# Kernel optimization log

Measured on AMD Instinct MI355X. Metric: run time of the kernel, lower is better.

The kernel has to match this reference:

```python
import jax, jax.numpy as jnp
import numpy as np

B, DIM, HW = 16, 256, 64      # input feature map
G, DH = 8, 64                 # offset_groups = heads = 8, dim_head = 64
DPG = DIM // G                # 32 channels per group
TP = 8                        # tile size: 8x8 grid of 8x8 tiles
DS = 4                        # downsample factor -> 2x2 offset grid per tile
CPB_DIM = DIM // 4            # 64, CPB mlp width
SCALE = DH ** -0.5


def _grid_sample(img, grid):
    # F.grid_sample, bilinear, zero padding, align_corners=False
    # img (N,C,H,W), grid (N,Ho,Wo,2) with last dim (x,y) in [-1,1]
    N, C, H, W = img.shape
    Ho, Wo = grid.shape[1:3]
    x = ((grid[..., 0] + 1.0) * W - 1.0) / 2.0
    y = ((grid[..., 1] + 1.0) * H - 1.0) / 2.0
    x0 = jnp.floor(x)
    y0 = jnp.floor(y)
    imgf = img.reshape(N, C, H * W)
    out = jnp.zeros((N, C, Ho * Wo), img.dtype)
    for dx, wx in ((0.0, x0 + 1.0 - x), (1.0, x - x0)):
        for dy, wy in ((0.0, y0 + 1.0 - y), (1.0, y - y0)):
            ix = x0 + dx
            iy = y0 + dy
            valid = (ix >= 0) & (ix < W) & (iy >= 0) & (iy < H)
            idx = (jnp.clip(iy, 0, H - 1) * W + jnp.clip(ix, 0, W - 1)).astype(jnp.int32)
            idxf = idx.reshape(N, Ho * Wo)
            g = jax.vmap(lambda im, ii: im[:, ii])(imgf, idxf)  # (N,C,HoWo)
            w = (wx * wy * valid).reshape(N, 1, Ho * Wo)
            out = out + g * w
    return out.reshape(N, C, Ho, Wo)


def _forward(x, ln_g, ln_b, wq, wk, wv, off_w1, off_b1, off_w2,
             cpb_w1, cpb_b1, cpb_w2, cpb_b2, cpb_w3, cpb_b3, wo, bo):
    Bb, C, H, W = x.shape
    # LayerNorm over channel dim (eps=1e-6)
    xt = jnp.moveaxis(x, 1, -1)
    mu = xt.mean(-1, keepdims=True)
    var = ((xt - mu) ** 2).mean(-1, keepdims=True)
    xt = (xt - mu) * jax.lax.rsqrt(var + 1e-6) * ln_g + ln_b
    x = jnp.moveaxis(xt, -1, 1)
    # patchify: (b c (i p) (j q)) -> ((i j b) c p q)  [vectorizes the 64-iter python loop]
    xp = x.reshape(Bb, C, 8, TP, 8, TP).transpose(2, 4, 0, 1, 3, 5).reshape(64 * Bb, C, TP, TP)
    N = 64 * Bb
    # grouped 1x1 to_q (groups = offset_groups)
    xg = xp.reshape(N, G, DPG, TP, TP)
    q = jnp.einsum('ngchw,goc->ngohw', xg, wq)          # (N,8,64,8,8)
    gq = q.reshape(N * G, DH, TP, TP)
    # offset net: depthwise conv k=6 s=4 p=1 -> GELU -> 1x1 -> tanh -> *offset_scale
    off = jax.lax.conv_general_dilated(gq, off_w1, (DS, DS), ((1, 1), (1, 1)),
                                       feature_group_count=DH)
    off = jax.nn.gelu(off + off_b1[None, :, None, None], approximate=False)
    off = jnp.tanh(jnp.einsum('nchw,oc->nohw', off, off_w2)) * float(DS)  # (N*G,2,2,2)
    # virtual sampling grid on the 2x2 offset grid, normalized by (size-1)
    r = jnp.arange(2, dtype=x.dtype)
    gx, gy = jnp.meshgrid(r, r, indexing='xy')
    vgrid = jnp.stack([gx, gy])[None] + off              # (N*G,2,2,2) ch=(x,y)
    vnorm = 2.0 * vgrid - 1.0                            # max(2-1,1)=1
    vgrid_s = jnp.moveaxis(vnorm, 1, -1)                 # (N*G,2,2,2) last=(x,y)
    kv = _grid_sample(xp.reshape(N * G, DPG, TP, TP), vgrid_s)   # (N*G,32,2,2)
    kvf = kv.reshape(N, G, DPG, 2, 2)
    k = jnp.einsum('ngchw,goc->ngohw', kvf, wk)          # (N,8,64,2,2)
    v = jnp.einsum('ngchw,goc->ngohw', kvf, wv)
    qh = q.transpose(0, 1, 3, 4, 2).reshape(N, G, TP * TP, DH) * SCALE
    kh = k.transpose(0, 1, 3, 4, 2).reshape(N, G, 4, DH)
    vh = v.transpose(0, 1, 3, 4, 2).reshape(N, G, 4, DH)
    sim = jnp.einsum('bhid,bhjd->bhij', qh, kh)          # (N,8,64,4)
    # continuous position bias (CPB)
    rq = jnp.arange(TP, dtype=x.dtype)
    qx, qy = jnp.meshgrid(rq, rq, indexing='xy')
    gridq = jnp.stack([qx, qy], -1).reshape(TP * TP, 2) * (2.0 / (TP - 1)) - 1.0
    pos = gridq[None, :, None, :] - vgrid_s.reshape(N * G, 1, 4, 2)  # (N*G,64,4,2)
    bz = jnp.sign(pos) * jnp.log1p(jnp.abs(pos))
    bz = jax.nn.relu(bz @ cpb_w1 + cpb_b1)
    bz = jax.nn.relu(bz @ cpb_w2 + cpb_b2)
    bz = (bz @ cpb_w3 + cpb_b3).reshape(N, G, TP * TP, 4)
    attn = jax.nn.softmax(sim + bz, axis=-1)
    out = jnp.einsum('bhij,bhjd->bhid', attn, vh)        # (N,8,64,64)
    out = out.transpose(0, 1, 3, 2).reshape(N, G * DH, TP, TP)
    out = jnp.einsum('nchw,oc->nohw', out, wo) + bo[None, :, None, None]
    # reassemble: ((i j b) c p q) -> (b c (i p) (j q))
    y = out.reshape(8, 8, Bb, C, TP, TP).transpose(2, 3, 0, 4, 1, 5).reshape(Bb, C, H, W)
    return y


def setup_inputs() -> dict:
    key = jax.random.key(0)
    ks = jax.random.split(key, 12)
    s = 0.05
    return {
        'x': jax.random.normal(ks[0], (B, DIM, HW, HW), jnp.float32),
        'ln_g': jnp.ones((DIM,), jnp.float32),
        'ln_b': jnp.zeros((DIM,), jnp.float32),
        'wq': jax.random.normal(ks[1], (G, DH, DPG), jnp.float32) * s,
        'wk': jax.random.normal(ks[2], (G, DH, DPG), jnp.float32) * s,
        'wv': jax.random.normal(ks[3], (G, DH, DPG), jnp.float32) * s,
        'off_w1': jax.random.normal(ks[4], (DH, 1, 6, 6), jnp.float32) * s,
        'off_b1': jnp.zeros((DH,), jnp.float32),
        'off_w2': jax.random.normal(ks[5], (2, DH), jnp.float32) * s,
        'cpb_w1': jax.random.normal(ks[6], (2, CPB_DIM), jnp.float32) * s,
        'cpb_b1': jnp.zeros((CPB_DIM,), jnp.float32),
        'cpb_w2': jax.random.normal(ks[7], (CPB_DIM, CPB_DIM), jnp.float32) * s,
        'cpb_b2': jnp.zeros((CPB_DIM,), jnp.float32),
        'cpb_w3': jax.random.normal(ks[8], (CPB_DIM, 1), jnp.float32) * s,
        'cpb_b3': jnp.zeros((1,), jnp.float32),
        'wo': jax.random.normal(ks[9], (DIM, G * DH), jnp.float32) * s,
        'bo': jnp.zeros((DIM,), jnp.float32),
    }


def reference(x, ln_g, ln_b, wq, wk, wv, off_w1, off_b1, off_w2,
              cpb_w1, cpb_b1, cpb_w2, cpb_b2, cpb_w3, cpb_b3, wo, bo):
    return _forward(x, ln_g, ln_b, wq, wk, wv, off_w1, off_b1, off_w2,
                    cpb_w1, cpb_b1, cpb_w2, cpb_b2, cpb_w3, cpb_b3, wo, bo)
```

## Files before the change

### kernel.cpp

```cpp
#include <hip/hip_runtime.h>
#include <math.h>


#define WS_VN  16777216
#define WS_WOT 16842752

typedef __attribute__((ext_vector_type(8))) short short8;
typedef __attribute__((ext_vector_type(4))) short short4b;
typedef __attribute__((ext_vector_type(4))) float f32x4;

__device__ __forceinline__ short f2bf(float f) {
  unsigned u = __builtin_bit_cast(unsigned, f);
  u += 0x7fff + ((u >> 16) & 1);
  return (short)(u >> 16);
}
__device__ __forceinline__ float bf2f(short h) {
  return __builtin_bit_cast(float, ((unsigned)(unsigned short)h) << 16);
}

__global__ __launch_bounds__(256) void k1_ln(const float* __restrict__ x,
    const float* __restrict__ ln_g, const float* __restrict__ ln_b,
    float* __restrict__ xn) {
  int blk = blockIdx.x;
  int b = blk >> 6, h = blk & 63;
  int t = threadIdx.x;
  int quarter = t >> 6, wcol = t & 63;
  const float* xrow = x + (size_t)b * (256 * 4096) + h * 64 + wcol;
  float vv[64];
  float s = 0.f, ss = 0.f;
#pragma unroll
  for (int i = 0; i < 64; ++i) {
    float v = xrow[(size_t)(quarter * 64 + i) * 4096];
    vv[i] = v; s += v; ss += v * v;
  }
  __shared__ float sm[4][64], sq[4][64], mu_s[64], rs_s[64];
  sm[quarter][wcol] = s; sq[quarter][wcol] = ss;
  __syncthreads();
  if (t < 64) {
    float S  = sm[0][t] + sm[1][t] + sm[2][t] + sm[3][t];
    float SS = sq[0][t] + sq[1][t] + sq[2][t] + sq[3][t];
    float mu = S * (1.f / 256.f);
    float var = SS * (1.f / 256.f) - mu * mu;
    mu_s[t] = mu;
    rs_s[t] = 1.f / sqrtf(var + 1e-6f);
  }
  __syncthreads();
  float mu = mu_s[wcol], rs = rs_s[wcol];
  int it = h >> 3, p = h & 7, jt = wcol >> 3, qq = wcol & 7;
  int n = (it * 8 + jt) * 16 + b;
  int pos = p * 8 + qq;
  float* xo = xn + (size_t)n * 16384 + pos * 256 + quarter * 64;
#pragma unroll
  for (int i = 0; i < 64; i += 4) {
    float4 o4;
    o4.x = (vv[i + 0] - mu) * rs * ln_g[quarter * 64 + i + 0] + ln_b[quarter * 64 + i + 0];
    o4.y = (vv[i + 1] - mu) * rs * ln_g[quarter * 64 + i + 1] + ln_b[quarter * 64 + i + 1];
    o4.z = (vv[i + 2] - mu) * rs * ln_g[quarter * 64 + i + 2] + ln_b[quarter * 64 + i + 2];
    o4.w = (vv[i + 3] - mu) * rs * ln_g[quarter * 64 + i + 3] + ln_b[quarter * 64 + i + 3];
    *(float4*)&xo[i] = o4;
  }
}

__global__ __launch_bounds__(256) void k0_cvt(const float* __restrict__ wo,
    short* __restrict__ woH, short* __restrict__ woL,
    const float* __restrict__ wq,
    short* __restrict__ wqH, short* __restrict__ wqL,
    const float* __restrict__ cw2, short* __restrict__ bfragG) {
  int blk = blockIdx.x;
  if (blk < 512) {
    int idx = blk * 256 + threadIdx.x;
    float v = wo[idx];
    short hi = f2bf(v);
    woH[idx] = hi;
    woL[idx] = f2bf(v - bf2f(hi));
  } else if (blk < 576) {
    int idx = (blk - 512) * 256 + threadIdx.x;
    float v = wq[idx];
    short hi = f2bf(v);
    wqH[idx] = hi;
    wqL[idx] = f2bf(v - bf2f(hi));
  } else {
    int t = threadIdx.x;
#pragma unroll
    for (int rep = 0; rep < 2; ++rep) {
      int slot = t + rep * 256;
      int combo = slot >> 6, ln = slot & 63;
      int kstep = combo >> 2, nt = combo & 3;
      int kbase = kstep * 32 + (ln >> 4) * 8;
      int ncol = nt * 16 + (ln & 15);
      short8 v;
#pragma unroll
      for (int jj = 0; jj < 8; ++jj) v[jj] = f2bf(cw2[(kbase + jj) * 64 + ncol]);
      *(short8*)&bfragG[slot * 8] = v;
    }
  }
}

__global__ __launch_bounds__(256, 4) void k2_qoff(const float* __restrict__ xn,
    const short* __restrict__ wqH, const short* __restrict__ wqL,
    const float* __restrict__ w1, const float* __restrict__ b1,
    const float* __restrict__ w2, short* __restrict__ qb,
    float* __restrict__ vn) {
  int blk = blockIdx.x;
  int n = blk >> 1, gh = blk & 1;
  int w = threadIdx.x >> 6;
  int lane = threadIdx.x & 63;
  int l15 = lane & 15, q4 = lane >> 4;
  __shared__ float qs[64][65];

  const float* w1c = w1 + lane * 36;
  float b1v = b1[lane];
  float w2a = w2[lane];
  float w2b = w2[64 + lane];
  int oy = w >> 1, ox = w & 1;
  int posc = w * 16 + l15;

  for (int gi = 0; gi < 4; ++gi) {
    int g = gh * 4 + gi;
    int ng = n * 8 + g;
    const float* xb = xn + (size_t)n * 16384 + posc * 256 + g * 32 + q4 * 8;
    float4 v0 = *(const float4*)xb;
    float4 v1 = *(const float4*)(xb + 4);
    float vj[8] = {v0.x, v0.y, v0.z, v0.w, v1.x, v1.y, v1.z, v1.w};
    short8 BH, BL;
#pragma unroll
    for (int j = 0; j < 8; ++j) {
      float v = vj[j];
      short hi = f2bf(v);
      BH[j] = hi;
      BL[j] = f2bf(v - bf2f(hi));
    }
    const short* wqHg = wqH + g * 2048;
    const short* wqLg = wqL + g * 2048;
    short* qrow = qb + ((size_t)(n * 64 + posc) * 512 + g * 64);
#pragma unroll
    for (int mt = 0; mt < 4; ++mt) {
      short8 AH = *(const short8*)&wqHg[(mt * 16 + l15) * 32 + q4 * 8];
      short8 AL = *(const short8*)&wqLg[(mt * 16 + l15) * 32 + q4 * 8];
      f32x4 acc = {0.f, 0.f, 0.f, 0.f};
      acc = __builtin_amdgcn_mfma_f32_16x16x32_bf16(AH, BH, acc, 0, 0, 0);
      acc = __builtin_amdgcn_mfma_f32_16x16x32_bf16(AL, BH, acc, 0, 0, 0);
      acc = __builtin_amdgcn_mfma_f32_16x16x32_bf16(AH, BL, acc, 0, 0, 0);
      int obase = mt * 16 + q4 * 4;
#pragma unroll
      for (int reg = 0; reg < 4; ++reg) qs[obase + reg][posc] = acc[reg];
      short4b qv;
#pragma unroll
      for (int reg = 0; reg < 4; ++reg) qv[reg] = f2bf(acc[reg]);
      *(short4b*)&qrow[obase] = qv;
    }
    __syncthreads();
    float a = 0.f;
#pragma unroll
    for (int ky = 0; ky < 6; ++ky) {
      int iy = oy * 4 - 1 + ky;
      if (iy < 0 || iy > 7) continue;
#pragma unroll
      for (int kx = 0; kx < 6; ++kx) {
        int ix = ox * 4 - 1 + kx;
        if (ix < 0 || ix > 7) continue;
        a += w1c[ky * 6 + kx] * qs[lane][iy * 8 + ix];
      }
    }
    a += b1v;
    a = 0.5f * a * (1.f + erff(a * 0.70710678118654752f));
    float p0 = w2a * a, p1 = w2b * a;
#pragma unroll
    for (int st = 1; st < 64; st <<= 1) {
      p0 += __shfl_xor(p0, st, 64);
      p1 += __shfl_xor(p1, st, 64);
    }
    if (lane == 0) {
      float offx = tanhf(p0) * 4.f;
      float offy = tanhf(p1) * 4.f;
      float2 o2;
      o2.x = 2.f * ((float)ox + offx) - 1.f;
      o2.y = 2.f * ((float)oy + offy) - 1.f;
      *(float2*)&vn[(size_t)ng * 8 + w * 2] = o2;
    }
    __syncthreads();
  }
}

__global__ __launch_bounds__(256, 3) void k3_attn(const float* __restrict__ xn,
    const float* __restrict__ wk, const float* __restrict__ wv,
    const float* __restrict__ vn, const short* __restrict__ bfragG,
    const float* __restrict__ cw1, const float* __restrict__ cb1,
    const float* __restrict__ cb2,
    const float* __restrict__ cw3, const float* __restrict__ cb3,
    short* __restrict__ qattB) {
  int w = threadIdx.x >> 6;
  int lane = threadIdx.x & 63;
  int ng = blockIdx.x * 4 + w;
  int n = ng >> 3, g = ng & 7;
  __shared__ alignas(16) float kvs[4][32][4];
  __shared__ alignas(16) float ks[4][64][4];
  __shared__ alignas(16) float vs[4][64][4];
  __shared__ alignas(16) short bfragLDS[512 * 8];
  __shared__ float biasS[4][4][64];

  {
    int t = threadIdx.x;
    *(short8*)&bfragLDS[t * 8]         = *(const short8*)&bfragG[t * 8];
    *(short8*)&bfragLDS[(t + 256) * 8] = *(const short8*)&bfragG[(t + 256) * 8];
  }

  const float* vp = vn + (size_t)ng * 8;
  float4 vp0 = *(const float4*)vp;
  float4 vp1 = *(const float4*)(vp + 4);
  float vx0 = vp0.x, vy0 = vp0.y, vx1 = vp0.z, vy1 = vp0.w;
  float vx2 = vp1.x, vy2 = vp1.y, vx3 = vp1.z, vy3 = vp1.w;
  {
    int c = lane & 31, s2 = lane >> 5;
    const float* tile = xn + (size_t)n * 16384 + g * 32 + c;
#pragma unroll
    for (int rep = 0; rep < 2; ++rep) {
      int s = s2 + 2 * rep;
      float vxs = (rep == 0) ? (s2 ? vx1 : vx0) : (s2 ? vx3 : vx2);
      float vys = (rep == 0) ? (s2 ? vy1 : vy0) : (s2 ? vy3 : vy2);
      float X = 4.f * vxs + 3.5f, Y = 4.f * vys + 3.5f;
      float x0f = floorf(X), y0f = floorf(Y);
      int x0 = (int)x0f, y0 = (int)y0f;
      float wx1 = X - x0f, wy1 = Y - y0f;
      float acc = 0.f;
      for (int dy = 0; dy < 2; ++dy) {
        int iy = y0 + dy;
        if (iy < 0 || iy > 7) continue;
        float wyv = dy ? wy1 : 1.f - wy1;
        for (int dx = 0; dx < 2; ++dx) {
          int ix = x0 + dx;
          if (ix < 0 || ix > 7) continue;
          float wxv = dx ? wx1 : 1.f - wx1;
          acc += tile[(iy * 8 + ix) * 256] * wxv * wyv;
        }
      }
      kvs[w][c][s] = acc;
    }
  }
  __syncthreads();
  {
    int d = lane;
    float ka0 = 0, ka1 = 0, ka2 = 0, ka3 = 0, va0 = 0, va1 = 0, va2 = 0, va3 = 0;
    const float4* wk4 = (const float4*)(wk + g * 2048 + d * 32);
    const float4* wv4 = (const float4*)(wv + g * 2048 + d * 32);
#pragma unroll
    for (int c4 = 0; c4 < 8; ++c4) {
      float4 a4 = wk4[c4], b4 = wv4[c4];
      float aw[4] = {a4.x, a4.y, a4.z, a4.w};
      float bw[4] = {b4.x, b4.y, b4.z, b4.w};
#pragma unroll
      for (int u = 0; u < 4; ++u) {
        float4 kv4 = *(const float4*)kvs[w][c4 * 4 + u];
        ka0 += aw[u] * kv4.x; ka1 += aw[u] * kv4.y;
        ka2 += aw[u] * kv4.z; ka3 += aw[u] * kv4.w;
        va0 += bw[u] * kv4.x; va1 += bw[u] * kv4.y;
        va2 += bw[u] * kv4.z; va3 += bw[u] * kv4.w;
      }
    }
    ks[w][d][0] = ka0; ks[w][d][1] = ka1; ks[w][d][2] = ka2; ks[w][d][3] = ka3;
    vs[w][d][0] = va0; vs[w][d][1] = va1; vs[w][d][2] = va2; vs[w][d][3] = va3;
  }
  __syncthreads();
  float sim0 = 0, sim1 = 0, sim2 = 0, sim3 = 0;
  short* qrow = qattB + ((size_t)(n * 64 + lane) * 512 + g * 64);
#pragma unroll 2
  for (int d8 = 0; d8 < 8; ++d8) {
    short8 q8 = *(const short8*)&qrow[d8 * 8];
#pragma unroll
    for (int j = 0; j < 8; ++j) {
      float qv = bf2f(q8[j]);
      float4 k4 = *(const float4*)ks[w][d8 * 8 + j];
      sim0 += qv * k4.x; sim1 += qv * k4.y; sim2 += qv * k4.z; sim3 += qv * k4.w;
    }
  }
  float logit0 = sim0 * 0.125f, logit1 = sim1 * 0.125f;
  float logit2 = sim2 * 0.125f, logit3 = sim3 * 0.125f;

  short8 bf[2][4];
#pragma unroll
  for (int kstep = 0; kstep < 2; ++kstep)
#pragma unroll
    for (int nt = 0; nt < 4; ++nt)
      bf[kstep][nt] = *(const short8*)&bfragLDS[((kstep * 4 + nt) * 64 + lane) * 8];
  int kcol = (lane >> 4) * 8;
  float c1x[16], c1y[16], c1b[16];
#pragma unroll
  for (int ks2 = 0; ks2 < 2; ++ks2)
#pragma unroll
    for (int jj = 0; jj < 8; ++jj) {
      int i = ks2 * 32 + kcol + jj;
      c1x[ks2 * 8 + jj] = cw1[i];
      c1y[ks2 * 8 + jj] = cw1[64 + i];
      c1b[ks2 * 8 + jj] = cb1[i];
    }
  int jme = lane & 15;
  float w3v[4], b2v[4];
#pragma unroll
  for (int nt = 0; nt < 4; ++nt) {
    w3v[nt] = cw3[nt * 16 + jme];
    b2v[nt] = cb2[nt * 16 + jme];
  }
  float gqx = (float)(jme & 7) * (2.f / 7.f) - 1.f;
  float yrow = (float)(jme >> 3);
#pragma unroll 1
  for (int s = 0; s < 4; ++s) {
    float vxs = (s == 0) ? vx0 : (s == 1) ? vx1 : (s == 2) ? vx2 : vx3;
    float vys = (s == 0) ? vy0 : (s == 1) ? vy1 : (s == 2) ? vy2 : vy3;
    float px = gqx - vxs;
    float tx = copysignf(log1pf(fabsf(px)), px);
    float pre[16];
#pragma unroll
    for (int t2 = 0; t2 < 16; ++t2) pre[t2] = fmaf(tx, c1x[t2], c1b[t2]);
#pragma unroll 1
    for (int mt4 = 0; mt4 < 4; ++mt4) {
      float gqy = (float)(mt4 * 2) * (2.f / 7.f) + yrow * (2.f / 7.f) - 1.f;
      float py = gqy - vys;
      float ty = copysignf(log1pf(fabsf(py)), py);
      short8 af[2];
#pragma unroll
      for (int ks2 = 0; ks2 < 2; ++ks2)
#pragma unroll
        for (int jj = 0; jj < 8; ++jj) {
          float h = fmaxf(fmaf(ty, c1y[ks2 * 8 + jj], pre[ks2 * 8 + jj]), 0.f);
          af[ks2][jj] = f2bf(h);
        }
      f32x4 a0 = {0,0,0,0}, a1 = {0,0,0,0}, a2 = {0,0,0,0}, a3 = {0,0,0,0};
      a0 = __builtin_amdgcn_mfma_f32_16x16x32_bf16(af[0], bf[0][0], a0, 0, 0, 0);
      a0 = __builtin_amdgcn_mfma_f32_16x16x32_bf16(af[1], bf[1][0], a0, 0, 0, 0);
      a1 = __builtin_amdgcn_mfma_f32_16x16x32_bf16(af[0], bf[0][1], a1, 0, 0, 0);
      a1 = __builtin_amdgcn_mfma_f32_16x16x32_bf16(af[1], bf[1][1], a1, 0, 0, 0);
      a2 = __builtin_amdgcn_mfma_f32_16x16x32_bf16(af[0], bf[0][2], a2, 0, 0, 0);
      a2 = __builtin_amdgcn_mfma_f32_16x16x32_bf16(af[1], bf[1][2], a2, 0, 0, 0);
      a3 = __builtin_amdgcn_mfma_f32_16x16x32_bf16(af[0], bf[0][3], a3, 0, 0, 0);
      a3 = __builtin_amdgcn_mfma_f32_16x16x32_bf16(af[1], bf[1][3], a3, 0, 0, 0);
      float part[4];
#pragma unroll
      for (int reg = 0; reg < 4; ++reg) {
        part[reg] = w3v[0] * fmaxf(a0[reg] + b2v[0], 0.f)
                  + w3v[1] * fmaxf(a1[reg] + b2v[1], 0.f)
                  + w3v[2] * fmaxf(a2[reg] + b2v[2], 0.f)
                  + w3v[3] * fmaxf(a3[reg] + b2v[3], 0.f);
      }
#pragma unroll
      for (int st = 1; st < 16; st <<= 1)
#pragma unroll
        for (int reg = 0; reg < 4; ++reg)
          part[reg] += __shfl_xor(part[reg], st, 64);
      if (jme == 0) {
        int posO = mt4 * 16 + (lane >> 4) * 4;
#pragma unroll
        for (int reg = 0; reg < 4; ++reg) biasS[w][s][posO + reg] = part[reg];
      }
    }
  }
  __syncthreads();
  float c3 = cb3[0];
  logit0 += biasS[w][0][lane] + c3;
  logit1 += biasS[w][1][lane] + c3;
  logit2 += biasS[w][2][lane] + c3;
  logit3 += biasS[w][3][lane] + c3;
  float m = fmaxf(fmaxf(logit0, logit1), fmaxf(logit2, logit3));
  float e0 = expf(logit0 - m), e1 = expf(logit1 - m);
  float e2 = expf(logit2 - m), e3 = expf(logit3 - m);
  float inv = 1.f / (e0 + e1 + e2 + e3);
  e0 *= inv; e1 *= inv; e2 *= inv; e3 *= inv;
#pragma unroll 2
  for (int d8 = 0; d8 < 8; ++d8) {
    short8 o8;
#pragma unroll
    for (int j = 0; j < 8; ++j) {
      float4 v4 = *(const float4*)vs[w][d8 * 8 + j];
      o8[j] = f2bf(e0 * v4.x + e1 * v4.y + e2 * v4.z + e3 * v4.w);
    }
    *(short8*)&qrow[d8 * 8] = o8;
  }
}

__global__ __launch_bounds__(256) void k4_mfma(const short* __restrict__ attB,
    const short* __restrict__ woH, const short* __restrict__ woL,
    const float* __restrict__ bo, float* __restrict__ y) {
  int blk = blockIdx.x;
  int b = blk & 15, it = (blk >> 4) & 7, p = blk >> 7;
  int wv = threadIdx.x >> 6;
  int lane = threadIdx.x & 63;
  int mr = lane & 15, kq = (lane >> 4) * 8;
  f32x4 acc[4][4];
#pragma unroll
  for (int mt = 0; mt < 4; ++mt)
#pragma unroll
    for (int nt = 0; nt < 4; ++nt) acc[mt][nt] = (f32x4){0.f, 0.f, 0.f, 0.f};
  int ncol0 = wv * 64 + mr;
  size_t arow[4];
#pragma unroll
  for (int mt = 0; mt < 4; ++mt) {
    int w0 = mt * 16 + mr;
    int jt = w0 >> 3, q = w0 & 7;
    arow[mt] = ((size_t)((it * 8 + jt) * 16 + b) * 64 + p * 8 + q) * 512;
  }
#pragma unroll 2
  for (int kst = 0; kst < 16; ++kst) {
    int k0 = kst * 32 + kq;
    short8 a[4];
#pragma unroll
    for (int mt = 0; mt < 4; ++mt)
      a[mt] = *(const short8*)&attB[arow[mt] + k0];
#pragma unroll
    for (int nt = 0; nt < 4; ++nt) {
      size_t off = (size_t)(ncol0 + nt * 16) * 512 + k0;
      short8 bhi = *(const short8*)&woH[off];
      short8 blo = *(const short8*)&woL[off];
#pragma unroll
      for (int mt = 0; mt < 4; ++mt) {
        acc[mt][nt] = __builtin_amdgcn_mfma_f32_16x16x32_bf16(a[mt], bhi, acc[mt][nt], 0, 0, 0);
        acc[mt][nt] = __builtin_amdgcn_mfma_f32_16x16x32_bf16(a[mt], blo, acc[mt][nt], 0, 0, 0);
      }
    }
  }
#pragma unroll
  for (int nt = 0; nt < 4; ++nt) {
    int o = wv * 64 + nt * 16 + mr;
    float bov = bo[o];
    size_t ybase = ((size_t)b * 256 + o) * 4096 + (it * 8 + p) * 64;
#pragma unroll
    for (int mt = 0; mt < 4; ++mt) {
      int w0 = mt * 16 + (lane >> 4) * 4;
      float4 o4;
      o4.x = acc[mt][nt][0] + bov;
      o4.y = acc[mt][nt][1] + bov;
      o4.z = acc[mt][nt][2] + bov;
      o4.w = acc[mt][nt][3] + bov;
      *(float4*)&y[ybase + w0] = o4;
    }
  }
}

extern "C" void kernel_launch(void* const* d_in, const int* in_sizes, int n_in,
                              void* d_out, int out_size, void* d_ws, size_t ws_size,
                              hipStream_t stream) {
  (void)in_sizes; (void)n_in; (void)out_size; (void)ws_size;
  const float* x    = (const float*)d_in[0];
  const float* ln_g = (const float*)d_in[1];
  const float* ln_b = (const float*)d_in[2];
  const float* wq   = (const float*)d_in[3];
  const float* wk   = (const float*)d_in[4];
  const float* wv   = (const float*)d_in[5];
  const float* ow1  = (const float*)d_in[6];
  const float* ob1  = (const float*)d_in[7];
  const float* ow2  = (const float*)d_in[8];
  const float* cw1  = (const float*)d_in[9];
  const float* cb1  = (const float*)d_in[10];
  const float* cw2  = (const float*)d_in[11];
  const float* cb2  = (const float*)d_in[12];
  const float* cw3  = (const float*)d_in[13];
  const float* cb3  = (const float*)d_in[14];
  const float* wo   = (const float*)d_in[15];
  const float* bo   = (const float*)d_in[16];
  float* y  = (float*)d_out;
  float* ws = (float*)d_ws;
  short* qattB = (short*)ws;
  float* vnb   = ws + WS_VN;
  short* woH   = (short*)(ws + WS_WOT);
  short* woL   = woH + 131072;
  short* wqH   = woL + 131072;
  short* wqL   = wqH + 16384;
  short* bfragG = wqL + 16384;
  float* xn = y;

  k0_cvt<<<577, 256, 0, stream>>>(wo, woH, woL, wq, wqH, wqL, cw2, bfragG);
  k1_ln<<<1024, 256, 0, stream>>>(x, ln_g, ln_b, xn);
  k2_qoff<<<2048, 256, 0, stream>>>(xn, wqH, wqL, ow1, ob1, ow2, qattB, vnb);
  k3_attn<<<2048, 256, 0, stream>>>(xn, wk, wv, vnb, bfragG, cw1, cb1, cb2,
                                    cw3, cb3, qattB);
  k4_mfma<<<1024, 256, 0, stream>>>(qattB, woH, woL, bo, y);
}
```

Measured before the change: 400.9 us.

## Split attention kernel into separate CPB bias kernel and attention kernel

Moves the continuous position bias MLP (MFMA-based) into its own kernel that writes per-head bias to workspace, and reduces the attention kernel to sampling, k/v projection, softmax and output. The split lowers LDS and register pressure in each kernel, so occupancy can rise (launch bounds 4 for attention). It costs an extra launch and a round trip of the bias buffer through global memory. The old fused kernel is kept as a fallback when the workspace is too small.

```diff
diff --git a/kernel.cpp b/kernel.cpp
--- a/kernel.cpp
+++ b/kernel.cpp
@@ -182,13 +182,103 @@
   }
 }
 
-__global__ __launch_bounds__(256, 3) void k3_attn(const float* __restrict__ xn,
-    const float* __restrict__ wk, const float* __restrict__ wv,
-    const float* __restrict__ vn, const short* __restrict__ bfragG,
+__global__ __launch_bounds__(256, 3) void k3a_cpb(const float* __restrict__ vn,
+    const short* __restrict__ bfragG,
     const float* __restrict__ cw1, const float* __restrict__ cb1,
     const float* __restrict__ cb2,
-    const float* __restrict__ cw3, const float* __restrict__ cb3,
-    short* __restrict__ qattB) {
+    const float* __restrict__ cw3, float* __restrict__ biasG) {
+  int w = threadIdx.x >> 6;
+  int lane = threadIdx.x & 63;
+  int ng = blockIdx.x * 4 + w;
+  const float* vp = vn + (size_t)ng * 8;
+  float4 vp0 = *(const float4*)vp;
+  float4 vp1 = *(const float4*)(vp + 4);
+  float vx0 = vp0.x, vy0 = vp0.y, vx1 = vp0.z, vy1 = vp0.w;
+  float vx2 = vp1.x, vy2 = vp1.y, vx3 = vp1.z, vy3 = vp1.w;
+
+  short8 bf[2][4];
+#pragma unroll
+  for (int kstep = 0; kstep < 2; ++kstep)
+#pragma unroll
+    for (int nt = 0; nt < 4; ++nt)
+      bf[kstep][nt] = *(const short8*)&bfragG[((kstep * 4 + nt) * 64 + lane) * 8];
+  int kcol = (lane >> 4) * 8;
+  float c1x[16], c1y[16], c1b[16];
+#pragma unroll
+  for (int ks2 = 0; ks2 < 2; ++ks2)
+#pragma unroll
+    for (int jj = 0; jj < 8; ++jj) {
+      int i = ks2 * 32 + kcol + jj;
+      c1x[ks2 * 8 + jj] = cw1[i];
+      c1y[ks2 * 8 + jj] = cw1[64 + i];
+      c1b[ks2 * 8 + jj] = cb1[i];
+    }
+  int jme = lane & 15;
+  float w3v[4], b2v[4];
+#pragma unroll
+  for (int nt = 0; nt < 4; ++nt) {
+    w3v[nt] = cw3[nt * 16 + jme];
+    b2v[nt] = cb2[nt * 16 + jme];
+  }
+  float gqx = (float)(jme & 7) * (2.f / 7.f) - 1.f;
+  float yrow = (float)(jme >> 3);
+#pragma unroll 1
+  for (int s = 0; s < 4; ++s) {
+    float vxs = (s == 0) ? vx0 : (s == 1) ? vx1 : (s == 2) ? vx2 : vx3;
+    float vys = (s == 0) ? vy0 : (s == 1) ? vy1 : (s == 2) ? vy2 : vy3;
+    float px = gqx - vxs;
+    float tx = copysignf(log1pf(fabsf(px)), px);
+    float pre[16];
+#pragma unroll
+    for (int t2 = 0; t2 < 16; ++t2) pre[t2] = fmaf(tx, c1x[t2], c1b[t2]);
+#pragma unroll 1
+    for (int mt4 = 0; mt4 < 4; ++mt4) {
+      float gqy = (float)(mt4 * 2) * (2.f / 7.f) + yrow * (2.f / 7.f) - 1.f;
+      float py = gqy - vys;
+      float ty = copysignf(log1pf(fabsf(py)), py);
+      short8 af[2];
+#pragma unroll
+      for (int ks2 = 0; ks2 < 2; ++ks2)
+#pragma unroll
+        for (int jj = 0; jj < 8; ++jj) {
+          float h = fmaxf(fmaf(ty, c1y[ks2 * 8 + jj], pre[ks2 * 8 + jj]), 0.f);
+          af[ks2][jj] = f2bf(h);
+        }
+      f32x4 a0 = {0,0,0,0}, a1 = {0,0,0,0}, a2 = {0,0,0,0}, a3 = {0,0,0,0};
+      a0 = __builtin_amdgcn_mfma_f32_16x16x32_bf16(af[0], bf[0][0], a0, 0, 0, 0);
+      a0 = __builtin_amdgcn_mfma_f32_16x16x32_bf16(af[1], bf[1][0], a0, 0, 0, 0);
+      a1 = __builtin_amdgcn_mfma_f32_16x16x32_bf16(af[0], bf[0][1], a1, 0, 0, 0);
+      a1 = __builtin_amdgcn_mfma_f32_16x16x32_bf16(af[1], bf[1][1], a1, 0, 0, 0);
+      a2 = __builtin_amdgcn_mfma_f32_16x16x32_bf16(af[0], bf[0][2], a2, 0, 0, 0);
+      a2 = __builtin_amdgcn_mfma_f32_16x16x32_bf16(af[1], bf[1][2], a2, 0, 0, 0);
+      a3 = __builtin_amdgcn_mfma_f32_16x16x32_bf16(af[0], bf[0][3], a3, 0, 0, 0);
+      a3 = __builtin_amdgcn_mfma_f32_16x16x32_bf16(af[1], bf[1][3], a3, 0, 0, 0);
+      float part[4];
+#pragma unroll
+      for (int reg = 0; reg < 4; ++reg) {
+        part[reg] = w3v[0] * fmaxf(a0[reg] + b2v[0], 0.f)
+                  + w3v[1] * fmaxf(a1[reg] + b2v[1], 0.f)
+                  + w3v[2] * fmaxf(a2[reg] + b2v[2], 0.f)
+                  + w3v[3] * fmaxf(a3[reg] + b2v[3], 0.f);
+      }
+#pragma unroll
+      for (int st = 1; st < 16; st <<= 1)
+#pragma unroll
+        for (int reg = 0; reg < 4; ++reg)
+          part[reg] += __shfl_xor(part[reg], st, 64);
+      if (jme == 0) {
+        int posO = mt4 * 16 + (lane >> 4) * 4;
+        float4 o4 = {part[0], part[1], part[2], part[3]};
+        *(float4*)&biasG[(size_t)ng * 256 + s * 64 + posO] = o4;
+      }
+    }
+  }
+}
+
+__global__ __launch_bounds__(256, 4) void k3b_attn(const float* __restrict__ xn,
+    const float* __restrict__ wk, const float* __restrict__ wv,
+    const float* __restrict__ vn, const float* __restrict__ biasG,
+    const float* __restrict__ cb3, short* __restrict__ qattB) {
   int w = threadIdx.x >> 6;
   int lane = threadIdx.x & 63;
   int ng = blockIdx.x * 4 + w;
@@ -196,14 +286,6 @@
   __shared__ alignas(16) float kvs[4][32][4];
   __shared__ alignas(16) float ks[4][64][4];
   __shared__ alignas(16) float vs[4][64][4];
-  __shared__ alignas(16) short bfragLDS[512 * 8];
-  __shared__ float biasS[4][4][64];
-
-  {
-    int t = threadIdx.x;
-    *(short8*)&bfragLDS[t * 8]         = *(const short8*)&bfragG[t * 8];
-    *(short8*)&bfragLDS[(t + 256) * 8] = *(const short8*)&bfragG[(t + 256) * 8];
-  }
 
   const float* vp = vn + (size_t)ng * 8;
   float4 vp0 = *(const float4*)vp;
@@ -275,6 +357,122 @@
   }
   float logit0 = sim0 * 0.125f, logit1 = sim1 * 0.125f;
   float logit2 = sim2 * 0.125f, logit3 = sim3 * 0.125f;
+  float c3 = cb3[0];
+  const float* bg = biasG + (size_t)ng * 256;
+  logit0 += bg[0 * 64 + lane] + c3;
+  logit1 += bg[1 * 64 + lane] + c3;
+  logit2 += bg[2 * 64 + lane] + c3;
+  logit3 += bg[3 * 64 + lane] + c3;
+  float m = fmaxf(fmaxf(logit0, logit1), fmaxf(logit2, logit3));
+  float e0 = expf(logit0 - m), e1 = expf(logit1 - m);
+  float e2 = expf(logit2 - m), e3 = expf(logit3 - m);
+  float inv = 1.f / (e0 + e1 + e2 + e3);
+  e0 *= inv; e1 *= inv; e2 *= inv; e3 *= inv;
+#pragma unroll 2
+  for (int d8 = 0; d8 < 8; ++d8) {
+    short8 o8;
+#pragma unroll
+    for (int j = 0; j < 8; ++j) {
+      float4 v4 = *(const float4*)vs[w][d8 * 8 + j];
+      o8[j] = f2bf(e0 * v4.x + e1 * v4.y + e2 * v4.z + e3 * v4.w);
+    }
+    *(short8*)&qrow[d8 * 8] = o8;
+  }
+}
+
+__global__ __launch_bounds__(256, 3) void k3_attn(const float* __restrict__ xn,
+    const float* __restrict__ wk, const float* __restrict__ wv,
+    const float* __restrict__ vn, const short* __restrict__ bfragG,
+    const float* __restrict__ cw1, const float* __restrict__ cb1,
+    const float* __restrict__ cb2,
+    const float* __restrict__ cw3, const float* __restrict__ cb3,
+    short* __restrict__ qattB) {
+  int w = threadIdx.x >> 6;
+  int lane = threadIdx.x & 63;
+  int ng = blockIdx.x * 4 + w;
+  int n = ng >> 3, g = ng & 7;
+  __shared__ alignas(16) float kvs[4][32][4];
+  __shared__ alignas(16) float ks[4][64][4];
+  __shared__ alignas(16) float vs[4][64][4];
+  __shared__ alignas(16) short bfragLDS[512 * 8];
+  __shared__ float biasS[4][4][64];
+
+  {
+    int t = threadIdx.x;
+    *(short8*)&bfragLDS[t * 8]         = *(const short8*)&bfragG[t * 8];
+    *(short8*)&bfragLDS[(t + 256) * 8] = *(const short8*)&bfragG[(t + 256) * 8];
+  }
+
+  const float* vp = vn + (size_t)ng * 8;
+  float4 vp0 = *(const float4*)vp;
+  float4 vp1 = *(const float4*)(vp + 4);
+  float vx0 = vp0.x, vy0 = vp0.y, vx1 = vp0.z, vy1 = vp0.w;
+  float vx2 = vp1.x, vy2 = vp1.y, vx3 = vp1.z, vy3 = vp1.w;
+  {
+    int c = lane & 31, s2 = lane >> 5;
+    const float* tile = xn + (size_t)n * 16384 + g * 32 + c;
+#pragma unroll
+    for (int rep = 0; rep < 2; ++rep) {
+      int s = s2 + 2 * rep;
+      float vxs = (rep == 0) ? (s2 ? vx1 : vx0) : (s2 ? vx3 : vx2);
+      float vys = (rep == 0) ? (s2 ? vy1 : vy0) : (s2 ? vy3 : vy2);
+      float X = 4.f * vxs + 3.5f, Y = 4.f * vys + 3.5f;
+      float x0f = floorf(X), y0f = floorf(Y);
+      int x0 = (int)x0f, y0 = (int)y0f;
+      float wx1 = X - x0f, wy1 = Y - y0f;
+      float acc = 0.f;
+      for (int dy = 0; dy < 2; ++dy) {
+        int iy = y0 + dy;
+        if (iy < 0 || iy > 7) continue;
+        float wyv = dy ? wy1 : 1.f - wy1;
+        for (int dx = 0; dx < 2; ++dx) {
+          int ix = x0 + dx;
+          if (ix < 0 || ix > 7) continue;
+          float wxv = dx ? wx1 : 1.f - wx1;
+          acc += tile[(iy * 8 + ix) * 256] * wxv * wyv;
+        }
+      }
+      kvs[w][c][s] = acc;
+    }
+  }
+  __syncthreads();
+  {
+    int d = lane;
+    float ka0 = 0, ka1 = 0, ka2 = 0, ka3 = 0, va0 = 0, va1 = 0, va2 = 0, va3 = 0;
+    const float4* wk4 = (const float4*)(wk + g * 2048 + d * 32);
+    const float4* wv4 = (const float4*)(wv + g * 2048 + d * 32);
+#pragma unroll
+    for (int c4 = 0; c4 < 8; ++c4) {
+      float4 a4 = wk4[c4], b4 = wv4[c4];
+      float aw[4] = {a4.x, a4.y, a4.z, a4.w};
+      float bw[4] = {b4.x, b4.y, b4.z, b4.w};
+#pragma unroll
+      for (int u = 0; u < 4; ++u) {
+        float4 kv4 = *(const float4*)kvs[w][c4 * 4 + u];
+        ka0 += aw[u] * kv4.x; ka1 += aw[u] * kv4.y;
+        ka2 += aw[u] * kv4.z; ka3 += aw[u] * kv4.w;
+        va0 += bw[u] * kv4.x; va1 += bw[u] * kv4.y;
+        va2 += bw[u] * kv4.z; va3 += bw[u] * kv4.w;
+      }
+    }
+    ks[w][d][0] = ka0; ks[w][d][1] = ka1; ks[w][d][2] = ka2; ks[w][d][3] = ka3;
+    vs[w][d][0] = va0; vs[w][d][1] = va1; vs[w][d][2] = va2; vs[w][d][3] = va3;
+  }
+  __syncthreads();
+  float sim0 = 0, sim1 = 0, sim2 = 0, sim3 = 0;
+  short* qrow = qattB + ((size_t)(n * 64 + lane) * 512 + g * 64);
+#pragma unroll 2
+  for (int d8 = 0; d8 < 8; ++d8) {
+    short8 q8 = *(const short8*)&qrow[d8 * 8];
+#pragma unroll
+    for (int j = 0; j < 8; ++j) {
+      float qv = bf2f(q8[j]);
+      float4 k4 = *(const float4*)ks[w][d8 * 8 + j];
+      sim0 += qv * k4.x; sim1 += qv * k4.y; sim2 += qv * k4.z; sim3 += qv * k4.w;
+    }
+  }
+  float logit0 = sim0 * 0.125f, logit1 = sim1 * 0.125f;
+  float logit2 = sim2 * 0.125f, logit3 = sim3 * 0.125f;
 
   short8 bf[2][4];
 #pragma unroll
@@ -437,7 +635,7 @@
 extern "C" void kernel_launch(void* const* d_in, const int* in_sizes, int n_in,
                               void* d_out, int out_size, void* d_ws, size_t ws_size,
                               hipStream_t stream) {
-  (void)in_sizes; (void)n_in; (void)out_size; (void)ws_size;
+  (void)in_sizes; (void)n_in; (void)out_size;
   const float* x    = (const float*)d_in[0];
   const float* ln_g = (const float*)d_in[1];
   const float* ln_b = (const float*)d_in[2];
@@ -464,12 +662,19 @@
   short* wqH   = woL + 131072;
   short* wqL   = wqH + 16384;
   short* bfragG = wqL + 16384;
+  float* biasG = (float*)(bfragG + 4096);
   float* xn = y;
+  const size_t needSplit = 76357632;
 
   k0_cvt<<<577, 256, 0, stream>>>(wo, woH, woL, wq, wqH, wqL, cw2, bfragG);
   k1_ln<<<1024, 256, 0, stream>>>(x, ln_g, ln_b, xn);
   k2_qoff<<<2048, 256, 0, stream>>>(xn, wqH, wqL, ow1, ob1, ow2, qattB, vnb);
-  k3_attn<<<2048, 256, 0, stream>>>(xn, wk, wv, vnb, bfragG, cw1, cb1, cb2,
-                                    cw3, cb3, qattB);
+  if (ws_size >= needSplit) {
+    k3a_cpb<<<2048, 256, 0, stream>>>(vnb, bfragG, cw1, cb1, cb2, cw3, biasG);
+    k3b_attn<<<2048, 256, 0, stream>>>(xn, wk, wv, vnb, biasG, cb3, qattB);
+  } else {
+    k3_attn<<<2048, 256, 0, stream>>>(xn, wk, wv, vnb, bfragG, cw1, cb1, cb2,
+                                      cw3, cb3, qattB);
+  }
   k4_mfma<<<1024, 256, 0, stream>>>(qattB, woH, woL, bo, y);
 }
```

Result: slower. 423.9 us (+5.7%).
